# Kernel optimization log

Measured on AMD Instinct MI355X. Metric: run time of the kernel, lower is better.

The kernel has to match this reference:

```python
import jax, jax.numpy as jnp
import numpy as np


def _cft_icft_matrices(n):
    # Continuous FT over t in [0,1) sampled at n points, frequencies = fftfreq(n, d=1/n).
    # CFT  : X(f) = integral x(t) e^{-2pi i f t} dt  ~=  (1/n) * sum_t x(t) e^{-2pi i f t}
    # ICFT : x(t) = integral X(f) e^{+2pi i f t} df  ~=  df   * sum_f X(f) e^{+2pi i f t}
    # The original module evaluates the ICFT on the fftshift-ed frequency grid while the
    # coefficients stay in fft (unshifted) index order; we reproduce that pairing.
    sr = float(n)
    t = jnp.arange(n, dtype=jnp.float32) / n                      # [n]
    f = jnp.fft.fftfreq(n, d=1.0 / sr).astype(jnp.float32)        # [n], fft order
    f_shift = jnp.fft.fftshift(f)                                 # [n], shifted order
    two_pi = jnp.float32(2.0 * np.pi)
    dt = jnp.float32(1.0 / n)
    df = jnp.float32(sr / n)  # frequency spacing = 1.0 for unit duration
    # E_cft: [n_freq, n_time], E_icft: [n_time, n_freq]
    E_cft = jnp.exp(-1j * two_pi * f[:, None] * t[None, :]).astype(jnp.complex64) * dt
    E_icft = jnp.exp(1j * two_pi * t[:, None] * f_shift[None, :]).astype(jnp.complex64) * df
    return E_cft, E_icft


def setup_inputs() -> dict:
    key = jax.random.key(0)
    k1, k2, k3 = jax.random.split(key, 3)
    B, Ci, Co, n, modes = 32, 64, 64, 4096, 64
    scale = 1.0 / (Ci * Co)
    x = jax.random.normal(k1, (B, Ci, n), dtype=jnp.float32)
    # weights1 = scale * rand(Ci, Co, modes, cfloat): uniform[0,1) real and imag parts
    w_real = scale * jax.random.uniform(k2, (Ci, Co, modes), dtype=jnp.float32)
    w_imag = scale * jax.random.uniform(k3, (Ci, Co, modes), dtype=jnp.float32)
    return {"x": x, "w_real": w_real, "w_imag": w_imag}


def reference(x, w_real, w_imag):
    B, Ci, n = x.shape
    Co, modes = w_real.shape[1], w_real.shape[2]
    E_cft, E_icft = _cft_icft_matrices(n)
    w = (w_real + 1j * w_imag).astype(jnp.complex64)              # [Ci, Co, modes]
    xc = x.astype(jnp.complex64)
    # Batched CFT over all (batch, channel) pairs as one complex GEMM.
    x_cft = jnp.einsum('bit,ft->bif', xc, E_cft)                  # [B, Ci, n]
    # Spectral linear transform on the lowest `modes` frequencies.
    low = jnp.einsum('bif,iof->bof', x_cft[:, :, :modes], w)      # [B, Co, modes]
    out_ft = jnp.zeros((B, Co, n), dtype=jnp.complex64).at[:, :, :modes].set(low)
    # Batched ICFT back to the time grid; module returns the real part.
    out = jnp.einsum('bof,tf->bot', out_ft, E_icft)               # [B, Co, n]
    return out.real
```

## Files before the change

### kernel.cpp

```cpp
#include <hip/hip_runtime.h>
#include <math.h>

#define NT 4096
#define MODES 64
#define ROWS 2048
#define TWO_PI 6.283185307179586f
#define PI_F 3.14159265358979f

static __device__ __forceinline__ void rotm(float& wr, float& wi, float sr, float si) {
  float nr = fmaf(wr, sr, -wi * si);
  float ni = fmaf(wr, si,  wi * sr);
  wr = nr; wi = ni;
}

__global__ __launch_bounds__(256) void cft_kernel(const float* __restrict__ x,
                                                  float2* __restrict__ xfp, int S) {
  __shared__ float4 xs4[32 * 65];
  const int tid = threadIdx.x;
  const int k0 = tid & 15;
  const int rg = tid >> 4;
  const int C = 512 / S;
  const int rowblk = (int)blockIdx.x / S;
  const int ts = (int)blockIdx.x % S;
  const int row0 = rowblk * 32;

  const int c4 = k0 & 3;
  const float p  = (c4 & 1) ? -1.f : 1.f;
  const float qc = (c4 == 0) ? 1.f : ((c4 == 2) ? -1.f : 0.f);
  const float rc = (c4 == 1) ? -1.f : ((c4 == 3) ? 1.f : 0.f);
  const int c8 = k0 & 7;
  float Aw, Bw;
  sincosf(-PI_F * (float)c8 * 0.25f, &Bw, &Aw);

  float st2r[4], st2i[4];
#pragma unroll
  for (int q = 0; q < 4; ++q) {
    const int k = k0 + 16 * q;
    sincosf(-TWO_PI * (float)(2 * k) / (float)NT, &st2i[q], &st2r[q]);
  }

  float ar[2][4] = {{0.f,0.f,0.f,0.f},{0.f,0.f,0.f,0.f}};
  float ai[2][4] = {{0.f,0.f,0.f,0.f},{0.f,0.f,0.f,0.f}};

  const float4* __restrict__ xg4 = (const float4*)x;
  const float* xsf = (const float*)xs4;

  for (int sub = 0; sub < C / 32; ++sub) {
    const int tl0 = ts * C + sub * 32;
    __syncthreads();
#pragma unroll
    for (int it = 0; it < 8; ++it) {
      const int idx = tid + it * 256;
      const int tlf = idx & 7;
      const int j = (idx >> 3) & 7;
      const int row = idx >> 6;
      float4 v = xg4[(size_t)(row0 + row) * (NT / 4) + j * 128 + (tl0 >> 2) + tlf];
      xs4[row * 65 + j * 8 + tlf] = v;
    }
    __syncthreads();
    float wAr[4], wAi[4], wBr[4], wBi[4];
#pragma unroll
    for (int q = 0; q < 4; ++q) {
      const int k = k0 + 16 * q;
      const int phA = (k * tl0) & (NT - 1);
      const int phB = (k * (tl0 + 1)) & (NT - 1);
      sincosf(-TWO_PI * (float)phA / (float)NT, &wAi[q], &wAr[q]);
      sincosf(-TWO_PI * (float)phB / (float)NT, &wBi[q], &wBr[q]);
    }
    for (int tt = 0; tt < 16; ++tt) {
#pragma unroll
      for (int par = 0; par < 2; ++par) {
        const int tl = 2 * tt + par;
        const float* wr = par ? wBr : wAr;
        const float* wi = par ? wBi : wAi;
#pragma unroll
        for (int rr = 0; rr < 2; ++rr) {
          const int row = rg * 2 + rr;
          const float* bp = xsf + row * 260 + tl;
          const float x0 = bp[0],   x1 = bp[32],  x2 = bp[64],  x3 = bp[96];
          const float x4 = bp[128], x5 = bp[160], x6 = bp[192], x7 = bp[224];
          const float ue = fmaf(p, x4, x0), ve = fmaf(p, x6, x2);
          const float Er = fmaf(qc, ve, ue), Ei = rc * ve;
          const float uo = fmaf(p, x5, x1), vo = fmaf(p, x7, x3);
          const float Or_ = fmaf(qc, vo, uo), Oi_ = rc * vo;
          float sr = fmaf(Aw, Or_, Er); sr = fmaf(-Bw, Oi_, sr);
          float si = fmaf(Aw, Oi_, Ei); si = fmaf( Bw, Or_, si);
#pragma unroll
          for (int q = 0; q < 4; ++q) {
            ar[rr][q] = fmaf(sr, wr[q], ar[rr][q]);
            ar[rr][q] = fmaf(-si, wi[q], ar[rr][q]);
            ai[rr][q] = fmaf(sr, wi[q], ai[rr][q]);
            ai[rr][q] = fmaf(si, wr[q], ai[rr][q]);
          }
        }
      }
#pragma unroll
      for (int q = 0; q < 4; ++q) {
        rotm(wAr[q], wAi[q], st2r[q], st2i[q]);
        rotm(wBr[q], wBi[q], st2r[q], st2i[q]);
      }
    }
  }
  const float dt = 1.0f / (float)NT;
#pragma unroll
  for (int rr = 0; rr < 2; ++rr) {
    const int row = row0 + rg * 2 + rr;
#pragma unroll
    for (int q = 0; q < 4; ++q) {
      xfp[((size_t)ts * ROWS + row) * MODES + k0 + 16 * q] =
          make_float2(ar[rr][q] * dt, ai[rr][q] * dt);
    }
  }
}

__global__ __launch_bounds__(256) void wt_reduce_kernel(
    const float* __restrict__ w_real, const float* __restrict__ w_imag,
    float* __restrict__ wrt, float* __restrict__ wit,
    const float4* __restrict__ xfp4, float2* __restrict__ xf_t, int S) {
  __shared__ float tile[64][65];
  __shared__ float2 rtile[8][65];
  const int tid = threadIdx.x;
  if (blockIdx.x < 128) {
    const int sel = blockIdx.x >> 6;
    const int io0 = ((int)blockIdx.x & 63) * 64;
    const float* __restrict__ src = sel ? w_imag : w_real;
    float* __restrict__ dst = sel ? wit : wrt;
#pragma unroll
    for (int j = 0; j < 4; ++j) {
      const int idx = tid + j * 256;
      const int r = idx >> 4;
      const int kq = idx & 15;
      float4 v = ((const float4*)src)[(size_t)(io0 + r) * 16 + kq];
      tile[r][4 * kq + 0] = v.x; tile[r][4 * kq + 1] = v.y;
      tile[r][4 * kq + 2] = v.z; tile[r][4 * kq + 3] = v.w;
    }
    __syncthreads();
#pragma unroll
    for (int j = 0; j < 16; ++j) {
      const int idx = tid + j * 256;
      const int k = idx >> 6;
      const int r = idx & 63;
      dst[(size_t)k * 4096 + io0 + r] = tile[r][k];
    }
  } else {
    const int blk = (int)blockIdx.x - 128;
    const int row0 = blk * 8;
    float4 acc = make_float4(0.f, 0.f, 0.f, 0.f);
    for (int s = 0; s < S; ++s) {
      float4 v = xfp4[((size_t)s * ROWS + row0) * 32 + tid];
      acc.x += v.x; acc.y += v.y; acc.z += v.z; acc.w += v.w;
    }
    const int r = tid >> 5;
    const int kp = tid & 31;
    rtile[r][2 * kp]     = make_float2(acc.x, acc.y);
    rtile[r][2 * kp + 1] = make_float2(acc.z, acc.w);
    __syncthreads();
#pragma unroll
    for (int jj = 0; jj < 2; ++jj) {
      const int e = tid + 256 * jj;
      const int k = e >> 3;
      const int rr = e & 7;
      xf_t[(size_t)k * ROWS + row0 + rr] = rtile[rr][k];
    }
  }
}

__global__ __launch_bounds__(256) void mix_kernel(const float* __restrict__ wrt,
                                                  const float* __restrict__ wit,
                                                  const float2* __restrict__ xf_t,
                                                  float2* __restrict__ yf_t) {
  __shared__ float2 wsc[4096];
  __shared__ float2 xsh[1024];
  const int k = blockIdx.x >> 1;
  const int bh = blockIdx.x & 1;
  const int tid = threadIdx.x;
#pragma unroll
  for (int j = 0; j < 4; ++j) {
    const int idx = tid + 256 * j;
    float4 vr = ((const float4*)(wrt + (size_t)k * 4096))[idx];
    float4 vi = ((const float4*)(wit + (size_t)k * 4096))[idx];
    wsc[4 * idx + 0] = make_float2(vr.x, vi.x);
    wsc[4 * idx + 1] = make_float2(vr.y, vi.y);
    wsc[4 * idx + 2] = make_float2(vr.z, vi.z);
    wsc[4 * idx + 3] = make_float2(vr.w, vi.w);
  }
#pragma unroll
  for (int j = 0; j < 2; ++j) {
    ((float4*)xsh)[tid + 256 * j] =
        ((const float4*)(xf_t + (size_t)k * ROWS + bh * 1024))[tid + 256 * j];
  }
  __syncthreads();
  const int o = tid & 63;
  const int bq = tid >> 6;
  float ar[4] = {0.f, 0.f, 0.f, 0.f};
  float ai[4] = {0.f, 0.f, 0.f, 0.f};
#pragma unroll 4
  for (int i = 0; i < 64; ++i) {
    const float2 w = wsc[i * 64 + o];
#pragma unroll
    for (int jb = 0; jb < 4; ++jb) {
      const float2 xv = xsh[(bq * 4 + jb) * 64 + i];
      ar[jb] = fmaf(xv.x, w.x, ar[jb]); ar[jb] = fmaf(-xv.y, w.y, ar[jb]);
      ai[jb] = fmaf(xv.x, w.y, ai[jb]); ai[jb] = fmaf( xv.y, w.x, ai[jb]);
    }
  }
#pragma unroll
  for (int jb = 0; jb < 4; ++jb) {
    yf_t[(size_t)k * ROWS + bh * 1024 + (bq * 4 + jb) * 64 + o] =
        make_float2(ar[jb], ai[jb]);
  }
}

__global__ __launch_bounds__(256) void icft_kernel(const float2* __restrict__ yf_t,
                                                   float* __restrict__ out) {
  __shared__ float2 ysh[4][66];
  const int rgrp = blockIdx.x >> 1;
  const int tc = blockIdx.x & 1;
  const int row0 = rgrp * 4;
  const int tid = threadIdx.x;
  {
    const int k = tid >> 2;
    const int r = tid & 3;
    ysh[r][k] = yf_t[(size_t)k * ROWS + row0 + r];
  }
  __syncthreads();
  const int tl = tc * 256 + tid;
  float stepr, stepi;
  sincosf(TWO_PI * (float)tl / (float)NT, &stepi, &stepr);
  float wr = 1.f, wi = 0.f;
  float Gr[8][4] = {{0.f}};
  float Gi[8][4] = {{0.f}};
  for (int m = 0; m < 8; ++m) {
#pragma unroll
    for (int cc = 0; cc < 8; ++cc) {
      const int k = 8 * m + cc;
#pragma unroll
      for (int r = 0; r < 4; ++r) {
        const float2 y = ysh[r][k];
        Gr[cc][r] = fmaf(y.x, wr, Gr[cc][r]);
        Gr[cc][r] = fmaf(-y.y, wi, Gr[cc][r]);
        if (cc != 0 && cc != 4) {
          Gi[cc][r] = fmaf(y.x, wi, Gi[cc][r]);
          Gi[cc][r] = fmaf(y.y, wr, Gi[cc][r]);
        }
      }
      rotm(wr, wi, stepr, stepi);
    }
  }
  const float KK = 0.7071067811865476f;
  const float sgn = (tl & 1) ? -1.f : 1.f;
#pragma unroll
  for (int r = 0; r < 4; ++r) {
    const float Ae = (Gr[0][r] + Gr[2][r]) + (Gr[4][r] + Gr[6][r]);
    const float Ao = (Gr[1][r] + Gr[3][r]) + (Gr[5][r] + Gr[7][r]);
    const float A2 = (Gr[0][r] - Gr[2][r]) + (Gr[4][r] - Gr[6][r]);
    const float B2 = (Gi[1][r] - Gi[3][r]) + (Gi[5][r] - Gi[7][r]);
    const float P  = Gr[0][r] - Gr[4][r];
    const float Qr = (Gr[1][r] - Gr[3][r]) - (Gr[5][r] - Gr[7][r]);
    const float R  = Gi[6][r] - Gi[2][r];
    const float Qi = (Gi[5][r] - Gi[1][r]) + (Gi[7][r] - Gi[3][r]);
    const float U = P + R, V = P - R;
    const float W1 = KK * (Qr + Qi), W2 = KK * (Qr - Qi);
    float* op = out + (size_t)(row0 + r) * NT + tl;
    op[0]    = sgn * (Ae + Ao);
    op[512]  = sgn * (U + W1);
    op[1024] = sgn * (A2 - B2);
    op[1536] = sgn * (V - W2);
    op[2048] = sgn * (Ae - Ao);
    op[2560] = sgn * (U - W1);
    op[3072] = sgn * (A2 + B2);
    op[3584] = sgn * (V + W2);
  }
}

extern "C" void kernel_launch(void* const* d_in, const int* in_sizes, int n_in,
                              void* d_out, int out_size, void* d_ws, size_t ws_size,
                              hipStream_t stream) {
  const float* x      = (const float*)d_in[0];
  const float* w_real = (const float*)d_in[1];
  const float* w_imag = (const float*)d_in[2];
  float* out = (float*)d_out;

  const size_t MB = (size_t)ROWS * MODES * sizeof(float2);
  int S = 16;
  while (S > 4 && (size_t)(S + 4) * MB > ws_size) S >>= 1;

  char* wsp = (char*)d_ws;
  float2* xfp  = (float2*)wsp;
  float2* xf_t = (float2*)(wsp + (size_t)S * MB);
  float2* yf_t = (float2*)(wsp + (size_t)(S + 1) * MB);
  float*  wrt  = (float*)(wsp + (size_t)(S + 2) * MB);
  float*  wit  = (float*)(wsp + (size_t)(S + 3) * MB);

  cft_kernel<<<64 * S, 256, 0, stream>>>(x, xfp, S);
  wt_reduce_kernel<<<384, 256, 0, stream>>>(w_real, w_imag, wrt, wit,
                                            (const float4*)xfp, xf_t, S);
  mix_kernel<<<128, 256, 0, stream>>>(wrt, wit, xf_t, yf_t);
  icft_kernel<<<1024, 256, 0, stream>>>(yf_t, out);
}
```

Before: 52.60 us.

## Fuse weight transpose into CFT and split-sum reduction into mix kernel

The weight-transpose blocks are appended to the CFT launch, and the partial-sum reduction over time splits moves into the mix kernel. This drops one kernel launch and the xf_t intermediate. The CFT partial output layout becomes mode-major so the mix kernel can read it directly. The CFT inner loop now reads shared memory as float2 pairs, and the mix kernel runs 512 smaller blocks of one row each. The trade-off is that every mix block reloads the full 64x64 weight slice for a quarter of the rows, and the reduction loads are strided.

```diff
diff --git a/kernel.cpp b/kernel.cpp
--- a/kernel.cpp
+++ b/kernel.cpp
@@ -13,10 +13,43 @@
   wr = nr; wi = ni;
 }
 
-__global__ __launch_bounds__(256) void cft_kernel(const float* __restrict__ x,
-                                                  float2* __restrict__ xfp, int S) {
-  __shared__ float4 xs4[32 * 65];
+__global__ __launch_bounds__(256) void cft_fused_kernel(
+    const float* __restrict__ x, float2* __restrict__ xfp,
+    const float* __restrict__ w_real, const float* __restrict__ w_imag,
+    float* __restrict__ wrt, float* __restrict__ wit, int S) {
+  __shared__ __align__(16) char smem[33280];
   const int tid = threadIdx.x;
+  const int nCft = 64 * S;
+
+  if ((int)blockIdx.x >= nCft) {
+    float (*tile)[65] = (float (*)[65])smem;
+    const int bx = (int)blockIdx.x - nCft;
+    const int sel = bx >> 6;
+    const int io0 = (bx & 63) * 64;
+    const float* __restrict__ src = sel ? w_imag : w_real;
+    float* __restrict__ dst = sel ? wit : wrt;
+#pragma unroll
+    for (int j = 0; j < 4; ++j) {
+      const int idx = tid + j * 256;
+      const int r = idx >> 4;
+      const int kq = idx & 15;
+      float4 v = ((const float4*)src)[(size_t)(io0 + r) * 16 + kq];
+      tile[r][4 * kq + 0] = v.x; tile[r][4 * kq + 1] = v.y;
+      tile[r][4 * kq + 2] = v.z; tile[r][4 * kq + 3] = v.w;
+    }
+    __syncthreads();
+#pragma unroll
+    for (int j = 0; j < 16; ++j) {
+      const int idx = tid + j * 256;
+      const int k = idx >> 6;
+      const int r = idx & 63;
+      dst[(size_t)k * 4096 + io0 + r] = tile[r][k];
+    }
+    return;
+  }
+
+  float4* xs4 = (float4*)smem;
+  const float* xsf = (const float*)smem;
   const int k0 = tid & 15;
   const int rg = tid >> 4;
   const int C = 512 / S;
@@ -43,7 +76,8 @@
   float ai[2][4] = {{0.f,0.f,0.f,0.f},{0.f,0.f,0.f,0.f}};
 
   const float4* __restrict__ xg4 = (const float4*)x;
-  const float* xsf = (const float*)xs4;
+  const float2* bp0 = (const float2*)(xsf + (rg * 2 + 0) * 260);
+  const float2* bp1 = (const float2*)(xsf + (rg * 2 + 1) * 260);
 
   for (int sub = 0; sub < C / 32; ++sub) {
     const int tl0 = ts * C + sub * 32;
@@ -54,8 +88,8 @@
       const int tlf = idx & 7;
       const int j = (idx >> 3) & 7;
       const int row = idx >> 6;
-      float4 v = xg4[(size_t)(row0 + row) * (NT / 4) + j * 128 + (tl0 >> 2) + tlf];
-      xs4[row * 65 + j * 8 + tlf] = v;
+      xs4[row * 65 + j * 8 + tlf] =
+          xg4[(size_t)(row0 + row) * (NT / 4) + j * 128 + (tl0 >> 2) + tlf];
     }
     __syncthreads();
     float wAr[4], wAi[4], wBr[4], wBi[4];
@@ -67,18 +101,29 @@
       sincosf(-TWO_PI * (float)phA / (float)NT, &wAi[q], &wAr[q]);
       sincosf(-TWO_PI * (float)phB / (float)NT, &wBi[q], &wBr[q]);
     }
+#pragma unroll 2
     for (int tt = 0; tt < 16; ++tt) {
+      float2 v0[8], v1[8];
+#pragma unroll
+      for (int j = 0; j < 8; ++j) {
+        v0[j] = bp0[j * 16 + tt];
+        v1[j] = bp1[j * 16 + tt];
+      }
 #pragma unroll
       for (int par = 0; par < 2; ++par) {
-        const int tl = 2 * tt + par;
-        const float* wr = par ? wBr : wAr;
-        const float* wi = par ? wBi : wAi;
+        const float* wrp = par ? wBr : wAr;
+        const float* wip = par ? wBi : wAi;
 #pragma unroll
         for (int rr = 0; rr < 2; ++rr) {
-          const int row = rg * 2 + rr;
-          const float* bp = xsf + row * 260 + tl;
-          const float x0 = bp[0],   x1 = bp[32],  x2 = bp[64],  x3 = bp[96];
-          const float x4 = bp[128], x5 = bp[160], x6 = bp[192], x7 = bp[224];
+          const float2* v = rr ? v1 : v0;
+          const float x0 = par ? v[0].y : v[0].x;
+          const float x1 = par ? v[1].y : v[1].x;
+          const float x2 = par ? v[2].y : v[2].x;
+          const float x3 = par ? v[3].y : v[3].x;
+          const float x4 = par ? v[4].y : v[4].x;
+          const float x5 = par ? v[5].y : v[5].x;
+          const float x6 = par ? v[6].y : v[6].x;
+          const float x7 = par ? v[7].y : v[7].x;
           const float ue = fmaf(p, x4, x0), ve = fmaf(p, x6, x2);
           const float Er = fmaf(qc, ve, ue), Ei = rc * ve;
           const float uo = fmaf(p, x5, x1), vo = fmaf(p, x7, x3);
@@ -87,10 +132,10 @@
           float si = fmaf(Aw, Oi_, Ei); si = fmaf( Bw, Or_, si);
 #pragma unroll
           for (int q = 0; q < 4; ++q) {
-            ar[rr][q] = fmaf(sr, wr[q], ar[rr][q]);
-            ar[rr][q] = fmaf(-si, wi[q], ar[rr][q]);
-            ai[rr][q] = fmaf(sr, wi[q], ai[rr][q]);
-            ai[rr][q] = fmaf(si, wr[q], ai[rr][q]);
+            ar[rr][q] = fmaf(sr, wrp[q], ar[rr][q]);
+            ar[rr][q] = fmaf(-si, wip[q], ar[rr][q]);
+            ai[rr][q] = fmaf(sr, wip[q], ai[rr][q]);
+            ai[rr][q] = fmaf(si, wrp[q], ai[rr][q]);
           }
         }
       }
@@ -102,77 +147,25 @@
     }
   }
   const float dt = 1.0f / (float)NT;
+  const size_t base = ((size_t)ts * 64 + rowblk) * 64;
 #pragma unroll
   for (int rr = 0; rr < 2; ++rr) {
-    const int row = row0 + rg * 2 + rr;
+    const int rl = rg * 2 + rr;
 #pragma unroll
     for (int q = 0; q < 4; ++q) {
-      xfp[((size_t)ts * ROWS + row) * MODES + k0 + 16 * q] =
+      xfp[(base + k0 + 16 * q) * 32 + rl] =
           make_float2(ar[rr][q] * dt, ai[rr][q] * dt);
     }
   }
 }
 
-__global__ __launch_bounds__(256) void wt_reduce_kernel(
-    const float* __restrict__ w_real, const float* __restrict__ w_imag,
-    float* __restrict__ wrt, float* __restrict__ wit,
-    const float4* __restrict__ xfp4, float2* __restrict__ xf_t, int S) {
-  __shared__ float tile[64][65];
-  __shared__ float2 rtile[8][65];
-  const int tid = threadIdx.x;
-  if (blockIdx.x < 128) {
-    const int sel = blockIdx.x >> 6;
-    const int io0 = ((int)blockIdx.x & 63) * 64;
-    const float* __restrict__ src = sel ? w_imag : w_real;
-    float* __restrict__ dst = sel ? wit : wrt;
-#pragma unroll
-    for (int j = 0; j < 4; ++j) {
-      const int idx = tid + j * 256;
-      const int r = idx >> 4;
-      const int kq = idx & 15;
-      float4 v = ((const float4*)src)[(size_t)(io0 + r) * 16 + kq];
-      tile[r][4 * kq + 0] = v.x; tile[r][4 * kq + 1] = v.y;
-      tile[r][4 * kq + 2] = v.z; tile[r][4 * kq + 3] = v.w;
-    }
-    __syncthreads();
-#pragma unroll
-    for (int j = 0; j < 16; ++j) {
-      const int idx = tid + j * 256;
-      const int k = idx >> 6;
-      const int r = idx & 63;
-      dst[(size_t)k * 4096 + io0 + r] = tile[r][k];
-    }
-  } else {
-    const int blk = (int)blockIdx.x - 128;
-    const int row0 = blk * 8;
-    float4 acc = make_float4(0.f, 0.f, 0.f, 0.f);
-    for (int s = 0; s < S; ++s) {
-      float4 v = xfp4[((size_t)s * ROWS + row0) * 32 + tid];
-      acc.x += v.x; acc.y += v.y; acc.z += v.z; acc.w += v.w;
-    }
-    const int r = tid >> 5;
-    const int kp = tid & 31;
-    rtile[r][2 * kp]     = make_float2(acc.x, acc.y);
-    rtile[r][2 * kp + 1] = make_float2(acc.z, acc.w);
-    __syncthreads();
-#pragma unroll
-    for (int jj = 0; jj < 2; ++jj) {
-      const int e = tid + 256 * jj;
-      const int k = e >> 3;
-      const int rr = e & 7;
-      xf_t[(size_t)k * ROWS + row0 + rr] = rtile[rr][k];
-    }
-  }
-}
-
-__global__ __launch_bounds__(256) void mix_kernel(const float* __restrict__ wrt,
-                                                  const float* __restrict__ wit,
-                                                  const float2* __restrict__ xf_t,
-                                                  float2* __restrict__ yf_t) {
+__global__ __launch_bounds__(256) void mix_kernel(
+    const float* __restrict__ wrt, const float* __restrict__ wit,
+    const float2* __restrict__ xfp, float2* __restrict__ yf_t, int S) {
   __shared__ float2 wsc[4096];
-  __shared__ float2 xsh[1024];
-  const int k = blockIdx.x >> 1;
-  const int bh = blockIdx.x & 1;
+  __shared__ float2 xsh[256];
+  const int k = blockIdx.x & 63;
+  const int bq = blockIdx.x >> 6;
   const int tid = threadIdx.x;
 #pragma unroll
   for (int j = 0; j < 4; ++j) {
@@ -184,31 +177,29 @@
     wsc[4 * idx + 2] = make_float2(vr.z, vi.z);
     wsc[4 * idx + 3] = make_float2(vr.w, vi.w);
   }
-#pragma unroll
-  for (int j = 0; j < 2; ++j) {
-    ((float4*)xsh)[tid + 256 * j] =
-        ((const float4*)(xf_t + (size_t)k * ROWS + bh * 1024))[tid + 256 * j];
+  {
+    const int R = bq * 256 + tid;
+    const int rowblk = R >> 5;
+    const int rl = R & 31;
+    float2 acc = make_float2(0.f, 0.f);
+    for (int s = 0; s < S; ++s) {
+      float2 v = xfp[(((size_t)s * 64 + rowblk) * 64 + k) * 32 + rl];
+      acc.x += v.x; acc.y += v.y;
+    }
+    xsh[tid] = acc;
   }
   __syncthreads();
   const int o = tid & 63;
-  const int bq = tid >> 6;
-  float ar[4] = {0.f, 0.f, 0.f, 0.f};
-  float ai[4] = {0.f, 0.f, 0.f, 0.f};
-#pragma unroll 4
+  const int bl = tid >> 6;
+  float accr = 0.f, acci = 0.f;
+#pragma unroll 8
   for (int i = 0; i < 64; ++i) {
+    const float2 xv = xsh[bl * 64 + i];
     const float2 w = wsc[i * 64 + o];
-#pragma unroll
-    for (int jb = 0; jb < 4; ++jb) {
-      const float2 xv = xsh[(bq * 4 + jb) * 64 + i];
-      ar[jb] = fmaf(xv.x, w.x, ar[jb]); ar[jb] = fmaf(-xv.y, w.y, ar[jb]);
-      ai[jb] = fmaf(xv.x, w.y, ai[jb]); ai[jb] = fmaf( xv.y, w.x, ai[jb]);
-    }
-  }
-#pragma unroll
-  for (int jb = 0; jb < 4; ++jb) {
-    yf_t[(size_t)k * ROWS + bh * 1024 + (bq * 4 + jb) * 64 + o] =
-        make_float2(ar[jb], ai[jb]);
-  }
+    accr = fmaf(xv.x, w.x, accr); accr = fmaf(-xv.y, w.y, accr);
+    acci = fmaf(xv.x, w.y, acci); acci = fmaf( xv.y, w.x, acci);
+  }
+  yf_t[(size_t)k * ROWS + bq * 256 + bl * 64 + o] = make_float2(accr, acci);
 }
 
 __global__ __launch_bounds__(256) void icft_kernel(const float2* __restrict__ yf_t,
@@ -287,14 +278,12 @@
 
   char* wsp = (char*)d_ws;
   float2* xfp  = (float2*)wsp;
-  float2* xf_t = (float2*)(wsp + (size_t)S * MB);
-  float2* yf_t = (float2*)(wsp + (size_t)(S + 1) * MB);
+  float2* yf_t = (float2*)(wsp + (size_t)S * MB);
   float*  wrt  = (float*)(wsp + (size_t)(S + 2) * MB);
   float*  wit  = (float*)(wsp + (size_t)(S + 3) * MB);
 
-  cft_kernel<<<64 * S, 256, 0, stream>>>(x, xfp, S);
-  wt_reduce_kernel<<<384, 256, 0, stream>>>(w_real, w_imag, wrt, wit,
-                                            (const float4*)xfp, xf_t, S);
-  mix_kernel<<<128, 256, 0, stream>>>(wrt, wit, xf_t, yf_t);
+  cft_fused_kernel<<<64 * S + 128, 256, 0, stream>>>(x, xfp, w_real, w_imag,
+                                                     wrt, wit, S);
+  mix_kernel<<<512, 256, 0, stream>>>(wrt, wit, xfp, yf_t, S);
   icft_kernel<<<1024, 256, 0, stream>>>(yf_t, out);
 }
```

New measurement: 49.66 us. 5.6% less time.
